# Kernel tuning notes

Hardware: AMD Instinct MI355X
Metric: run time of the kernel (lower is better)

Reference implementation:

```python
import jax, jax.numpy as jnp
import numpy as np

N_HEAD = 16
HEAD_DIM = 64


def _shift(BD):
    # BD: [b, n, L, 2L] -> [b, n, L, L] (Transformer-XL left-shift trick)
    b, n, L, _ = BD.shape
    BD = jnp.pad(BD, ((0, 0), (0, 0), (0, 0), (0, 1)))          # [b,n,L,2L+1]
    BD = BD.reshape(b, n, 2 * L + 1, L)[:, :, :-1]              # [b,n,2L,L]
    BD = BD.reshape(b, n, L, 2 * L)[:, :, :, L:]                # [b,n,L,L]
    return BD


def _transpose_shift(E):
    # E: [b, n, L, 2L] -> [b, n, L, L]
    b, n, L, _ = E.shape
    E = jnp.pad(E, ((0, 0), (0, 0), (0, 0), (0, 1)))            # [b,n,L,2L+1]
    E = E.reshape(b, n, 2 * L + 1, L)                           # [b,n,2L+1,L]
    E = E[:, :, 1::2, :]                                        # rows 1,3,...,2L-1 -> [b,n,L,L]
    return E


def setup_inputs() -> dict:
    key = jax.random.key(0)
    ks = jax.random.split(key, 6)
    B, L, D = 4, 1024, 1024
    return {
        "x": jax.random.normal(ks[0], (B, L, D), jnp.float32),
        "pos_embed": jax.random.normal(ks[1], (2 * L, HEAD_DIM), jnp.float32),
        "W_qkv": jax.random.normal(ks[2], (D, 3 * D), jnp.float32) * (1.0 / np.sqrt(D)),
        "b_qkv": jax.random.normal(ks[3], (3 * D,), jnp.float32) * 0.01,
        "r_r_bias": jax.random.normal(ks[4], (N_HEAD, HEAD_DIM), jnp.float32) * 0.02,
        "r_w_bias": jax.random.normal(ks[5], (N_HEAD, HEAD_DIM), jnp.float32) * 0.02,
    }


def reference(x, pos_embed, W_qkv, b_qkv, r_r_bias, r_w_bias):
    b, L, d_model = x.shape
    scale = jnp.sqrt(jnp.asarray(HEAD_DIM, x.dtype))

    qkv = x @ W_qkv + b_qkv                                      # [b,L,3D]
    q, k, v = jnp.split(qkv, 3, axis=-1)

    def split_heads(t):  # [b,L,D] -> [b,n,L,hd]
        return t.reshape(b, L, N_HEAD, HEAD_DIM).transpose(0, 2, 1, 3)

    q, k, v = split_heads(q), split_heads(k), split_heads(v)

    rw_head_q = q + r_r_bias[None, :, None, :]
    AC = jnp.einsum('bnqd,bnkd->bnqk', rw_head_q, k)             # [b,n,L,L]
    D_ = jnp.einsum('nd,ld->nl', r_w_bias, pos_embed)[None, :, None, :]  # [1,n,1,2L]
    B_ = jnp.einsum('bnqd,ld->bnql', q, pos_embed)               # [b,n,L,2L]
    E_ = jnp.einsum('bnqd,ld->bnql', k, pos_embed)               # [b,n,L,2L]

    BDE = _shift(B_ + D_) + _transpose_shift(E_)
    attn = jax.nn.softmax((AC + BDE) / scale, axis=-1)

    out = jnp.einsum('bnqk,bnkd->bnqd', attn, v)                 # [b,n,L,hd]
    out = out.transpose(0, 2, 1, 3).reshape(b, L, d_model)       # merge heads
    return out
```

## Files before the change

kernel.cpp:

```cpp
#include <hip/hip_runtime.h>
#include <math.h>

typedef unsigned short u16;
typedef unsigned int u32;
typedef __attribute__((ext_vector_type(8))) short bf16x8;
typedef __attribute__((ext_vector_type(4))) float f32x4;

#define AS1 __attribute__((address_space(1)))
#define AS3 __attribute__((address_space(3)))

static __device__ __forceinline__ u16 f2b(float f) {
  u32 u = __float_as_uint(f);
  return (u16)((u + 0x7FFFu + ((u >> 16) & 1u)) >> 16);
}
static __device__ __forceinline__ u16 f2b_fast(float f) {
  return (u16)((__float_as_uint(f) + 0x8000u) >> 16);
}
static __device__ __forceinline__ float b2f(u16 b) {
  return __uint_as_float(((u32)b) << 16);
}

__global__ __launch_bounds__(256) void prep(
    const float* __restrict__ x, const float* __restrict__ W,
    const float* __restrict__ P,
    u16* __restrict__ xb, u16* __restrict__ Wt, u16* __restrict__ Pb)
{
  __shared__ u16 sT[64 * 68];
  const int bid = blockIdx.x, t = threadIdx.x;
  if (bid < 4096) {
    const size_t base = (size_t)bid * 1024 + t * 4;
    const float4 v = *(const float4*)(x + base);
    const u32 lo = (u32)f2b(v.x) | ((u32)f2b(v.y) << 16);
    const u32 hi = (u32)f2b(v.z) | ((u32)f2b(v.w) << 16);
    *(uint2*)(xb + base) = make_uint2(lo, hi);
  } else if (bid < 4224) {
    const size_t base = (size_t)(bid - 4096) * 1024 + t * 4;
    const float4 v = *(const float4*)(P + base);
    const u32 lo = (u32)f2b(v.x) | ((u32)f2b(v.y) << 16);
    const u32 hi = (u32)f2b(v.z) | ((u32)f2b(v.w) << 16);
    *(uint2*)(Pb + base) = make_uint2(lo, hi);
  } else if (bid < 4992) {
    const int tb = bid - 4224;
    const int tk = tb / 48, tn = tb % 48;
    const int k0 = tk * 64, n0 = tn * 64;
#pragma unroll
    for (int it = 0; it < 4; ++it) {
      const int c = it * 256 + t;
      const int r = c >> 4, c4 = (c & 15) << 2;
      const float4 v = *(const float4*)(W + (size_t)(k0 + r) * 3072 + n0 + c4);
      sT[(c4 + 0) * 68 + r] = f2b(v.x);
      sT[(c4 + 1) * 68 + r] = f2b(v.y);
      sT[(c4 + 2) * 68 + r] = f2b(v.z);
      sT[(c4 + 3) * 68 + r] = f2b(v.w);
    }
    __syncthreads();
#pragma unroll
    for (int it = 0; it < 4; ++it) {
      const int c = it * 256 + t;
      const int rr = c >> 4, k4 = (c & 15) << 2;
      const uint2 rv = *(const uint2*)(sT + rr * 68 + k4);
      *(uint2*)(Wt + (size_t)(n0 + rr) * 1024 + k0 + k4) = rv;
    }
  } else {
    if (t < 64) Pb[2048 * 64 + t] = f2b(P[2047 * 64 + t]);
  }
}

__global__ __launch_bounds__(256, 3) void qkv_gemm(
    const u16* __restrict__ xb, const u16* __restrict__ Wt,
    const float* __restrict__ bq,
    u16* __restrict__ Qh, u16* __restrict__ Kh, u16* __restrict__ Vt)
{
  __shared__ u16 smem[20480];
  u16* const sA = smem;
  u16* const sB = smem + 8192;
  u16* const T  = smem;
  u16* const Tv = smem;
  const int t = threadIdx.x;
  const int lane = t & 63, w = t >> 6;
  const int l = lane & 15, ql = lane >> 4;
  const int wm = w & 1, wn = w >> 1;
  const int vid = blockIdx.x;
  const int xcd = vid & 7, jj = vid >> 3;
  const int n0 = (xcd * 3 + (jj % 3)) * 128;
  const int m0 = (jj / 3) * 128;

  f32x4 acc[4][4];
#pragma unroll
  for (int i = 0; i < 4; ++i)
#pragma unroll
    for (int j = 0; j < 4; ++j) acc[i][j] = (f32x4){0.f, 0.f, 0.f, 0.f};

  for (int k0 = 0; k0 < 1024; k0 += 64) {
    __syncthreads();
#pragma unroll
    for (int j = 0; j < 4; ++j) {
      const int ii = w * 4 + j;
      const int m = ii * 8 + (lane >> 3);
      const int q8 = (lane & 7) ^ (m & 7);
      __builtin_amdgcn_global_load_lds(
          (const AS1 u32*)(xb + (size_t)(m0 + m) * 1024 + k0 + q8 * 8),
          (AS3 u32*)(sA + ii * 512), 16, 0, 0);
      __builtin_amdgcn_global_load_lds(
          (const AS1 u32*)(Wt + (size_t)(n0 + m) * 1024 + k0 + q8 * 8),
          (AS3 u32*)(sB + ii * 512), 16, 0, 0);
    }
    __syncthreads();
#pragma unroll
    for (int ks = 0; ks < 2; ++ks) {
      bf16x8 a[4], b[4];
#pragma unroll
      for (int mt = 0; mt < 4; ++mt) {
        const int m = wm * 64 + mt * 16 + l;
        a[mt] = *(const bf16x8*)(sA + m * 64 + (((ks * 4 + ql) ^ (m & 7)) * 8));
      }
#pragma unroll
      for (int nt = 0; nt < 4; ++nt) {
        const int nn = wn * 64 + nt * 16 + l;
        b[nt] = *(const bf16x8*)(sB + nn * 64 + (((ks * 4 + ql) ^ (nn & 7)) * 8));
      }
#pragma unroll
      for (int mt = 0; mt < 4; ++mt)
#pragma unroll
        for (int nt = 0; nt < 4; ++nt)
          acc[mt][nt] = __builtin_amdgcn_mfma_f32_16x16x32_bf16(
              a[mt], b[nt], acc[mt][nt], 0, 0, 0);
    }
  }

  const int which = n0 >> 10;
  const int qbase = m0 & 1023;
  const int bb = m0 >> 10;
  const int h0 = (n0 & 1023) >> 6;
  __syncthreads();
  if (which < 2) {
#pragma unroll
    for (int nt = 0; nt < 4; ++nt) {
      const int col = wn * 64 + nt * 16 + l;
      const float bias = bq[n0 + col];
#pragma unroll
      for (int mt = 0; mt < 4; ++mt)
#pragma unroll
        for (int rg = 0; rg < 4; ++rg)
          T[(wm * 64 + mt * 16 + ql * 4 + rg) * 136 + col] =
              f2b(acc[mt][nt][rg] + bias);
    }
    __syncthreads();
    u16* const dst = which ? Kh : Qh;
#pragma unroll
    for (int h = 0; h < 2; ++h) {
      const size_t bnoff = ((size_t)(bb * 16 + h0 + h)) << 16;
#pragma unroll
      for (int it = 0; it < 4; ++it) {
        const int c = it * 256 + t;
        const int r = c >> 3, d8 = (c & 7) * 8;
        const uint4 v = *(const uint4*)(T + r * 136 + h * 64 + d8);
        *(uint4*)(dst + bnoff + ((size_t)(qbase + r) << 6) + d8) = v;
      }
    }
  } else {
#pragma unroll
    for (int nt = 0; nt < 4; ++nt) {
      const int col = wn * 64 + nt * 16 + l;
      const float bias = bq[n0 + col];
#pragma unroll
      for (int mt = 0; mt < 4; ++mt) {
        const u32 lo = (u32)f2b(acc[mt][nt][0] + bias) |
                       ((u32)f2b(acc[mt][nt][1] + bias) << 16);
        const u32 hi = (u32)f2b(acc[mt][nt][2] + bias) |
                       ((u32)f2b(acc[mt][nt][3] + bias) << 16);
        *(uint2*)(Tv + col * 136 + wm * 64 + mt * 16 + ql * 4) =
            make_uint2(lo, hi);
      }
    }
    __syncthreads();
#pragma unroll
    for (int h = 0; h < 2; ++h) {
      const size_t bnoff = ((size_t)(bb * 16 + h0 + h)) << 16;
#pragma unroll
      for (int it = 0; it < 4; ++it) {
        const int c = it * 256 + t;
        const int dr = c >> 4, q8 = (c & 15) * 8;
        const uint4 v = *(const uint4*)(Tv + (h * 64 + dr) * 136 + q8);
        *(uint4*)(Vt + bnoff + ((size_t)dr << 10) + qbase + q8) = v;
      }
    }
  }
}

__global__ __launch_bounds__(512, 4) void rel_attn(
    const u16* __restrict__ Qh, const u16* __restrict__ Kh,
    const u16* __restrict__ Vt, const u16* __restrict__ Pb,
    const float* __restrict__ rrb, const float* __restrict__ rwb,
    float* __restrict__ out)
{
  __shared__ u16 smem[36864];
  u16* const sK    = smem;
  u16* const sVT   = smem + 8192;
  u16* const sPr   = smem + 16384;
  u16* const sProb = smem + 32768;
  u16* const sU    = smem;
  u16* const sW    = smem + 16384;

  const int t = threadIdx.x;
  const int lane = t & 63, w = t >> 6;
  const int l = lane & 15, ql = lane >> 4;
  const int vid = blockIdx.x;
  const int qt = vid >> 6, bn = vid & 63;
  const int n = bn & 15, bb = bn >> 4;
  const size_t hoff = (size_t)bn << 16;
  const int q0 = qt << 7;
  const int bz = 7 - w;

#pragma unroll
  for (int it = 0; it < 2; ++it) {
    const int c = it * 512 + t;
    const int i = c >> 3, ch = c & 7;
    const int d8 = ch * 8;
    const uint4 qv = *(const uint4*)(Qh + hoff + ((size_t)(q0 + i) << 6) + d8);
    const uint4 kv = *(const uint4*)(Kh + hoff + ((size_t)(q0 + i) << 6) + d8);
    const u16* qp = (const u16*)&qv;
    const u16* kp = (const u16*)&kv;
    u16 uo[8], wo[8];
#pragma unroll
    for (int e = 0; e < 8; ++e) {
      const float rv = rrb[n * 64 + d8 + e];
      const float wv = rwb[n * 64 + d8 + e];
      const float qf = b2f(qp[e]), kf = b2f(kp[e]);
      uo[e] = f2b(qf + rv);
      wo[e] = f2b(qf + wv + kf);
    }
    const int pos = i * 64 + ((ch ^ (i & 7)) * 8);
    *(uint4*)(sU + pos) = *(const uint4*)uo;
    *(uint4*)(sW + pos) = *(const uint4*)wo;
  }
  __syncthreads();

  bf16x8 au[2], aw[2];
#pragma unroll
  for (int ks = 0; ks < 2; ++ks) {
    const int row = w * 16 + l;
    const int off = row * 64 + (((ks * 4 + ql) ^ (row & 7)) * 8);
    au[ks] = *(const bf16x8*)(sU + off);
    aw[ks] = *(const bf16x8*)(sW + off);
  }
  __syncthreads();

  {
    const int m = w * 8 + (lane >> 3);
    const int q8 = (lane & 7) ^ (m & 7);
    __builtin_amdgcn_global_load_lds(
        (const AS1 u32*)(Kh + hoff + ((size_t)m << 6) + q8 * 8),
        (AS3 u32*)(sK + w * 512), 16, 0, 0);
    __builtin_amdgcn_global_load_lds(
        (const AS1 u32*)(Vt + hoff + ((size_t)m << 10) + q8 * 8),
        (AS3 u32*)(sVT + w * 512), 16, 0, 0);
    const int lbase0 = 897 - q0;
    const int rb0 = (896 - q0) & 255;
#pragma unroll
    for (int j = 0; j < 3; ++j) {
      const int ii = w * 3 + j;
      const int mm = ii * 8 + (lane >> 3);
      const int qq = (lane & 7) ^ (mm & 7);
      __builtin_amdgcn_global_load_lds(
          (const AS1 u32*)(Pb + ((size_t)(lbase0 + mm) << 6) + qq * 8),
          (AS3 u32*)(sPr + ((rb0 + ii * 8) & 255) * 64), 16, 0, 0);
    }
  }

  const f32x4 Z0 = (f32x4){0.f, 0.f, 0.f, 0.f};
  f32x4 o[4];
  float lrun[4];
#pragma unroll
  for (int ii = 0; ii < 4; ++ii) {
    o[ii] = (f32x4){0.f, 0.f, 0.f, 0.f};
    lrun[ii] = 0.f;
  }

  for (int k0 = 0; k0 < 1024; k0 += 64) {
    const int cb = (k0 >> 6) & 1;
    const int rb = (896 + k0 - q0) & 255;
    __syncthreads();

    if (k0 < 960) {
      const int kn = k0 + 64;
      const int m = w * 8 + (lane >> 3);
      const int q8 = (lane & 7) ^ (m & 7);
      __builtin_amdgcn_global_load_lds(
          (const AS1 u32*)(Kh + hoff + ((size_t)(kn + m) << 6) + q8 * 8),
          (AS3 u32*)(sK + (cb ^ 1) * 4096 + w * 512), 16, 0, 0);
      __builtin_amdgcn_global_load_lds(
          (const AS1 u32*)(Vt + hoff + ((size_t)m << 10) + kn + q8 * 8),
          (AS3 u32*)(sVT + (cb ^ 1) * 4096 + w * 512), 16, 0, 0);
      __builtin_amdgcn_global_load_lds(
          (const AS1 u32*)(Pb + ((size_t)(897 + kn + 128 - q0 + m) << 6) + q8 * 8),
          (AS3 u32*)(sPr + ((rb + 192 + w * 8) & 255) * 64), 16, 0, 0);
    }

    const u16* const cK = sK + cb * 4096;
    const u16* const cV = sVT + cb * 4096;

    f32x4 z1[4], z2[5];
    __builtin_amdgcn_s_setprio(1);
#pragma unroll
    for (int ks = 0; ks < 2; ++ks) {
#pragma unroll
      for (int nt = 0; nt < 4; ++nt) {
        const int row = nt * 16 + l;
        const bf16x8 bk =
            *(const bf16x8*)(cK + row * 64 + (((ks * 4 + ql) ^ (row & 7)) * 8));
        z1[nt] = __builtin_amdgcn_mfma_f32_16x16x32_bf16(
            au[ks], bk, ks ? z1[nt] : Z0, 0, 0, 0);
      }
#pragma unroll
      for (int rt = 0; rt < 5; ++rt) {
        const int row = (bz + rt) * 16 + l;
        const bf16x8 bp = *(const bf16x8*)(
            sPr + ((rb + row) & 255) * 64 + (((ks * 4 + ql) ^ (row & 7)) * 8));
        z2[rt] = __builtin_amdgcn_mfma_f32_16x16x32_bf16(
            aw[ks], bp, ks ? z2[rt] : Z0, 0, 0, 0);
      }
    }
    __builtin_amdgcn_s_setprio(0);

    float p[4][4];
#pragma unroll
    for (int ii = 0; ii < 4; ++ii) {
      const int ci = 15 - ql * 4 - ii;
      const int src = (lane & 48) | ((l + ci) & 15);
      const bool wrap = l < ci;
#pragma unroll
      for (int jt = 0; jt < 4; ++jt) {
        const float val = wrap ? z2[jt + 1][ii] : z2[jt][ii];
        const float g = __shfl(val, src, 64);
        const float pv =
            __builtin_amdgcn_exp2f((z1[jt][ii] + g) * 0.18033688011112042f);
        p[ii][jt] = pv;
        lrun[ii] += pv;
      }
    }

#pragma unroll
    for (int ks = 0; ks < 2; ++ks) {
#pragma unroll
      for (int ii = 0; ii < 4; ++ii) {
        const int r = w * 16 + ql * 4 + ii;
        const int sw2 = (r & 3) ^ ((r >> 2) & 3);
#pragma unroll
        for (int jh = 0; jh < 2; ++jh) {
          const int ch = jh * 2 + (l >> 3);
          sProb[r * 32 + ((ch ^ sw2) * 8) + (l & 7)] =
              f2b_fast(p[ii][ks * 2 + jh]);
        }
      }
      bf16x8 bv[4];
#pragma unroll
      for (int dt = 0; dt < 4; ++dt) {
        const int row = dt * 16 + l;
        bv[dt] =
            *(const bf16x8*)(cV + row * 64 + (((ks * 4 + ql) ^ (row & 7)) * 8));
      }
      __builtin_amdgcn_s_setprio(1);
      {
        const int ar = w * 16 + l;
        const bf16x8 ap = *(const bf16x8*)(
            sProb + ar * 32 + ((ql ^ ((ar & 3) ^ ((ar >> 2) & 3))) * 8));
#pragma unroll
        for (int dt = 0; dt < 4; ++dt)
          o[dt] = __builtin_amdgcn_mfma_f32_16x16x32_bf16(
              ap, bv[dt], o[dt], 0, 0, 0);
      }
      __builtin_amdgcn_s_setprio(0);
    }
  }

#pragma unroll
  for (int ii = 0; ii < 4; ++ii) {
    float ls = lrun[ii];
    ls += __shfl_xor(ls, 1);
    ls += __shfl_xor(ls, 2);
    ls += __shfl_xor(ls, 4);
    ls += __shfl_xor(ls, 8);
    const float inv = 1.f / ls;
    const int q = q0 + w * 16 + ql * 4 + ii;
#pragma unroll
    for (int dt = 0; dt < 4; ++dt)
      out[((size_t)(bb * 1024 + q) << 10) + (n << 6) + dt * 16 + l] =
          o[dt][ii] * inv;
  }
}

extern "C" void kernel_launch(void* const* d_in, const int* in_sizes, int n_in,
                              void* d_out, int out_size, void* d_ws, size_t ws_size,
                              hipStream_t stream) {
  const float* x  = (const float*)d_in[0];
  const float* P  = (const float*)d_in[1];
  const float* Wq = (const float*)d_in[2];
  const float* bq = (const float*)d_in[3];
  const float* rr = (const float*)d_in[4];
  const float* rw = (const float*)d_in[5];
  float* out = (float*)d_out;

  char* ws = (char*)d_ws;
  u16* xb = (u16*)(ws);
  u16* Wt = (u16*)(ws + 8388608);
  u16* Pb = (u16*)(ws + 14680064);
  u16* Qh = (u16*)(ws + 14946304);
  u16* Kh = (u16*)(ws + 23334912);
  u16* Vt = (u16*)(ws + 31723520);

  prep<<<4993, 256, 0, stream>>>(x, Wq, P, xb, Wt, Pb);
  qkv_gemm<<<768, 256, 0, stream>>>(xb, Wt, bq, Qh, Kh, Vt);
  rel_attn<<<512, 512, 0, stream>>>(Qh, Kh, Vt, Pb, rr, rw, out);
}
```

Baseline: 170.5 us.

## Double-buffer QKV GEMM LDS tiles with K-step 32 and prefetch

Restructures the QKV projection GEMM main loop into a two-stage LDS double buffer. K slices are cut from 64 to 32 so both buffers fit in the existing shared allocation, and the XOR swizzle is rewritten for the narrower rows. The next tile's global-to-LDS load is issued before the current tile's MFMAs, which drops one barrier per iteration and overlaps memory with compute. MFMA sections are also wrapped in s_setprio. The trade-off is twice as many loop iterations, each with less work per barrier.

New measurement: 164.0 us. -3.8%, faster.

```diff
diff --git a/kernel.cpp b/kernel.cpp
--- a/kernel.cpp
+++ b/kernel.cpp
@@ -80,6 +80,8 @@
   const int lane = t & 63, w = t >> 6;
   const int l = lane & 15, ql = lane >> 4;
   const int wm = w & 1, wn = w >> 1;
+  const int srow = lane >> 2;
+  const int sc   = lane & 3;
   const int vid = blockIdx.x;
   const int xcd = vid & 7, jj = vid >> 3;
   const int n0 = (xcd * 3 + (jj % 3)) * 128;
@@ -91,41 +93,62 @@
 #pragma unroll
     for (int j = 0; j < 4; ++j) acc[i][j] = (f32x4){0.f, 0.f, 0.f, 0.f};
 
-  for (int k0 = 0; k0 < 1024; k0 += 64) {
+#pragma unroll
+  for (int j = 0; j < 2; ++j) {
+    const int ii = w * 2 + j;
+    const int m = ii * 16 + srow;
+    const int cs = sc ^ ((m & 3) ^ ((m >> 2) & 1));
+    __builtin_amdgcn_global_load_lds(
+        (const AS1 u32*)(xb + (size_t)(m0 + m) * 1024 + cs * 8),
+        (AS3 u32*)(sA + ii * 512), 16, 0, 0);
+    __builtin_amdgcn_global_load_lds(
+        (const AS1 u32*)(Wt + (size_t)(n0 + m) * 1024 + cs * 8),
+        (AS3 u32*)(sB + ii * 512), 16, 0, 0);
+  }
+
+  for (int it = 0; it < 32; ++it) {
+    const int cur = it & 1;
     __syncthreads();
-#pragma unroll
-    for (int j = 0; j < 4; ++j) {
-      const int ii = w * 4 + j;
-      const int m = ii * 8 + (lane >> 3);
-      const int q8 = (lane & 7) ^ (m & 7);
-      __builtin_amdgcn_global_load_lds(
-          (const AS1 u32*)(xb + (size_t)(m0 + m) * 1024 + k0 + q8 * 8),
-          (AS3 u32*)(sA + ii * 512), 16, 0, 0);
-      __builtin_amdgcn_global_load_lds(
-          (const AS1 u32*)(Wt + (size_t)(n0 + m) * 1024 + k0 + q8 * 8),
-          (AS3 u32*)(sB + ii * 512), 16, 0, 0);
-    }
-    __syncthreads();
-#pragma unroll
-    for (int ks = 0; ks < 2; ++ks) {
-      bf16x8 a[4], b[4];
-#pragma unroll
-      for (int mt = 0; mt < 4; ++mt) {
-        const int m = wm * 64 + mt * 16 + l;
-        a[mt] = *(const bf16x8*)(sA + m * 64 + (((ks * 4 + ql) ^ (m & 7)) * 8));
-      }
-#pragma unroll
-      for (int nt = 0; nt < 4; ++nt) {
-        const int nn = wn * 64 + nt * 16 + l;
-        b[nt] = *(const bf16x8*)(sB + nn * 64 + (((ks * 4 + ql) ^ (nn & 7)) * 8));
-      }
-#pragma unroll
-      for (int mt = 0; mt < 4; ++mt)
-#pragma unroll
-        for (int nt = 0; nt < 4; ++nt)
-          acc[mt][nt] = __builtin_amdgcn_mfma_f32_16x16x32_bf16(
-              a[mt], b[nt], acc[mt][nt], 0, 0, 0);
-    }
+
+    if (it < 31) {
+      const int kn = (it + 1) * 32;
+#pragma unroll
+      for (int j = 0; j < 2; ++j) {
+        const int ii = w * 2 + j;
+        const int m = ii * 16 + srow;
+        const int cs = sc ^ ((m & 3) ^ ((m >> 2) & 1));
+        __builtin_amdgcn_global_load_lds(
+            (const AS1 u32*)(xb + (size_t)(m0 + m) * 1024 + kn + cs * 8),
+            (AS3 u32*)(sA + (cur ^ 1) * 4096 + ii * 512), 16, 0, 0);
+        __builtin_amdgcn_global_load_lds(
+            (const AS1 u32*)(Wt + (size_t)(n0 + m) * 1024 + kn + cs * 8),
+            (AS3 u32*)(sB + (cur ^ 1) * 4096 + ii * 512), 16, 0, 0);
+      }
+    }
+
+    const u16* const cA = sA + cur * 4096;
+    const u16* const cB = sB + cur * 4096;
+    bf16x8 a[4], b[4];
+#pragma unroll
+    for (int mt = 0; mt < 4; ++mt) {
+      const int m = wm * 64 + mt * 16 + l;
+      a[mt] = *(const bf16x8*)(cA + m * 32 +
+                               ((ql ^ ((m & 3) ^ ((m >> 2) & 1))) * 8));
+    }
+#pragma unroll
+    for (int nt = 0; nt < 4; ++nt) {
+      const int nn = wn * 64 + nt * 16 + l;
+      b[nt] = *(const bf16x8*)(cB + nn * 32 +
+                               ((ql ^ ((nn & 3) ^ ((nn >> 2) & 1))) * 8));
+    }
+    __builtin_amdgcn_s_setprio(1);
+#pragma unroll
+    for (int mt = 0; mt < 4; ++mt)
+#pragma unroll
+      for (int nt = 0; nt < 4; ++nt)
+        acc[mt][nt] = __builtin_amdgcn_mfma_f32_16x16x32_bf16(
+            a[mt], b[nt], acc[mt][nt], 0, 0, 0);
+    __builtin_amdgcn_s_setprio(0);
   }
 
   const int which = n0 >> 10;
```
